# Optimization experiments

Measured on AMD Instinct MI355X. Metric: run time of the kernel, lower is better.

Reference implementation:

```python
import jax, jax.numpy as jnp
import numpy as np

B, S, D = 4, 2048, 1024

def setup_inputs() -> dict:
    key = jax.random.key(0)
    kx, kq, kk, kv = jax.random.split(key, 4)
    glorot = (6.0 / (D + D)) ** 0.5
    return {
        "x": jax.random.normal(kx, (B, S, D), dtype=jnp.float32),
        "Wq": jax.random.uniform(kq, (D, D), jnp.float32, -glorot, glorot),
        "Wk": jax.random.uniform(kk, (D, D), jnp.float32, -glorot, glorot),
        "Wv": jax.random.uniform(kv, (D, D), jnp.float32, -glorot, glorot),
    }

def reference(x, Wq, Wk, Wv):
    # q,k,v: [B,S,D]
    q = jnp.einsum("bsd,de->bse", x, Wq)
    k = jnp.einsum("bsd,de->bse", x, Wk)
    v = jnp.einsum("bsd,de->bse", x, Wv)
    scale = jnp.sqrt(jnp.asarray(q.shape[-1], q.dtype))
    scores = jnp.einsum("bqd,bkd->bqk", q, k) / scale  # [B,S,S]
    w = jax.nn.softmax(scores, axis=-1)
    return jnp.einsum("bqk,bkd->bqd", w, v)
```

## Files before the change

kernel.cpp:

```cpp
#include <hip/hip_runtime.h>
#include <hip/hip_bf16.h>


typedef _Float16 half_t;
typedef _Float16 half8 __attribute__((ext_vector_type(8)));
typedef _Float16 half4v __attribute__((ext_vector_type(4)));
typedef float f32x4 __attribute__((ext_vector_type(4)));

__device__ __forceinline__ void load16_to_lds(const half_t* g, half_t* l) {
  __builtin_amdgcn_global_load_lds(
      (const __attribute__((address_space(1))) void*)g,
      (__attribute__((address_space(3))) void*)l, 16, 0, 0);
}

__global__ __launch_bounds__(512, 2) void qkvt_gemm8(
    const half_t* __restrict__ xh, const half_t* __restrict__ wt,
    half_t* __restrict__ qk, half_t* __restrict__ vtg) {
  __shared__ __align__(16) half_t As[2][256 * 64];
  __shared__ __align__(16) half_t Bs[2][256 * 64];

  int b = blockIdx.x;
  const half_t* A; const half_t* Bm; half_t* C;
  int ldc, m0, n0;
  if (b < 256) {
    A = xh; Bm = wt; C = qk; ldc = 2048;
    m0 = (b >> 3) * 256; n0 = (b & 7) * 256;
  } else {
    b -= 256;
    A = wt + (size_t)2 * 1024 * 1024; Bm = xh; C = vtg; ldc = 8192;
    m0 = (b >> 5) * 256; n0 = (b & 31) * 256;
  }

  const int t     = threadIdx.x;
  const int lane  = t & 63;
  const int wave  = t >> 6;
  const int wr128 = (wave >> 2) * 128;
  const int wc64  = (wave & 3) * 64;
  const int lm    = lane & 15;
  const int lq    = lane >> 4;
  const int pos0  = (lq ^ (lm & 7)) * 8;
  const int pos1  = ((4 + lq) ^ (lm & 7)) * 8;
  const int t8    = t * 8;

  const int trow = t >> 3;
  const int tchk = (t & 7) ^ (trow & 7);
  const half_t* gA0 = A  + (size_t)(m0 + trow) * 1024 + tchk * 8;
  const half_t* gB0 = Bm + (size_t)(n0 + trow) * 1024 + tchk * 8;

  f32x4 acc[8][4] = {};
  half8 va[4][2], vb0[2][2], vb1[2][2];

#define ST_A(buf, h, kt) do {                                                  \
    load16_to_lds(gA0 + (size_t)((h)*128) * 1024 + (size_t)(kt) * 64,          \
                  &As[buf][(h)*128*64] + t8);                                  \
    load16_to_lds(gA0 + (size_t)((h)*128+64) * 1024 + (size_t)(kt) * 64,       \
                  &As[buf][((h)*128+64)*64] + t8);                             \
  } while (0)
#define ST_B(buf, h, kt) do {                                                  \
    load16_to_lds(gB0 + (size_t)((h)*128) * 1024 + (size_t)(kt) * 64,          \
                  &Bs[buf][(h)*128*64] + t8);                                  \
    load16_to_lds(gB0 + (size_t)((h)*128+64) * 1024 + (size_t)(kt) * 64,       \
                  &Bs[buf][((h)*128+64)*64] + t8);                             \
  } while (0)
#define RD_A(buf, mh) do {                                                     \
    _Pragma("unroll") for (int m = 0; m < 4; ++m) {                            \
      const int ar = wr128 + (mh)*64 + m * 16 + lm;                            \
      va[m][0] = *(const half8*)&As[buf][ar * 64 + pos0];                      \
      va[m][1] = *(const half8*)&As[buf][ar * 64 + pos1];                      \
    } } while (0)
#define RD_B(buf, nh, vb) do {                                                 \
    _Pragma("unroll") for (int n = 0; n < 2; ++n) {                            \
      const int br = wc64 + (nh)*32 + n * 16 + lm;                             \
      vb[n][0] = *(const half8*)&Bs[buf][br * 64 + pos0];                      \
      vb[n][1] = *(const half8*)&Bs[buf][br * 64 + pos1];                      \
    } } while (0)
#define MF_Q(mh, nh, vb) do {                                                  \
    _Pragma("unroll") for (int kk = 0; kk < 2; ++kk)                           \
    _Pragma("unroll") for (int m = 0; m < 4; ++m)                              \
    _Pragma("unroll") for (int n = 0; n < 2; ++n)                              \
      acc[(mh)*4+m][(nh)*2+n] = __builtin_amdgcn_mfma_f32_16x16x32_f16(        \
          va[m][kk], vb[n][kk], acc[(mh)*4+m][(nh)*2+n], 0, 0, 0);             \
  } while (0)
#define LGKM0 asm volatile("s_waitcnt lgkmcnt(0)" ::: "memory")
#define BAR   __builtin_amdgcn_s_barrier()
#define PRIO1 __builtin_amdgcn_s_setprio(1)
#define PRIO0 __builtin_amdgcn_s_setprio(0)

  ST_A(0, 0, 0); ST_A(0, 1, 0);
  ST_B(0, 0, 0); ST_B(0, 1, 0);
  ST_B(1, 0, 1); ST_B(1, 1, 1);
  asm volatile("s_waitcnt vmcnt(4)" ::: "memory");
  BAR;

#pragma unroll 1
  for (int i = 0; i < 8; ++i) {
    const int st1 = (2 * i + 1 < 15) ? 2 * i + 1 : 15;
    const int st2 = (2 * i + 2 < 15) ? 2 * i + 2 : 15;
    const int st3 = (2 * i + 3 < 15) ? 2 * i + 3 : 15;
    RD_A(0, 0); RD_B(0, 0, vb0);
    ST_A(1, 0, st1);
    asm volatile("s_waitcnt lgkmcnt(8)" ::: "memory");
    BAR; LGKM0;
    PRIO1; MF_Q(0, 0, vb0); PRIO0;
    BAR;
    RD_B(0, 1, vb1);
    ST_A(1, 1, st1);
    BAR; LGKM0;
    PRIO1; MF_Q(0, 1, vb1); PRIO0;
    BAR;
    RD_A(0, 1);
    ST_B(0, 0, st2);
    BAR; LGKM0;
    PRIO1; MF_Q(1, 0, vb0); PRIO0;
    BAR;
    ST_B(0, 1, st2);
    BAR; LGKM0;
    PRIO1; MF_Q(1, 1, vb1); PRIO0;
    asm volatile("s_waitcnt vmcnt(4)" ::: "memory");
    BAR;
    RD_A(1, 0); RD_B(1, 0, vb0);
    ST_A(0, 0, st2);
    asm volatile("s_waitcnt lgkmcnt(8)" ::: "memory");
    BAR; LGKM0;
    PRIO1; MF_Q(0, 0, vb0); PRIO0;
    BAR;
    RD_B(1, 1, vb1);
    ST_A(0, 1, st2);
    BAR; LGKM0;
    PRIO1; MF_Q(0, 1, vb1); PRIO0;
    BAR;
    RD_A(1, 1);
    ST_B(1, 0, st3);
    BAR; LGKM0;
    PRIO1; MF_Q(1, 0, vb0); PRIO0;
    BAR;
    ST_B(1, 1, st3);
    BAR; LGKM0;
    PRIO1; MF_Q(1, 1, vb1); PRIO0;
    asm volatile("s_waitcnt vmcnt(4)" ::: "memory");
    BAR;
  }

#pragma unroll
  for (int m = 0; m < 8; ++m)
#pragma unroll
    for (int n = 0; n < 4; ++n) {
      const int col = n0 + wc64 + n * 16 + lm;
#pragma unroll
      for (int r = 0; r < 4; ++r) {
        const int row = m0 + wr128 + m * 16 + lq * 4 + r;
        C[(size_t)row * ldc + col] = (half_t)acc[m][n][r];
      }
    }
#undef ST_A
#undef ST_B
#undef RD_A
#undef RD_B
#undef MF_Q
#undef LGKM0
#undef BAR
#undef PRIO1
#undef PRIO0
}

__global__ __launch_bounds__(256) void scores_gemm(
    const half_t* __restrict__ qk, half_t* __restrict__ sc,
    float* __restrict__ lpart) {
  __shared__ __align__(16) half_t As[128 * 64];
  __shared__ __align__(16) half_t Bs[128 * 64];

  const int z  = blockIdx.z;
  const int m0 = blockIdx.y * 128;
  const int n0 = blockIdx.x * 128;
  const half_t* A  = qk + (size_t)z * 2048 * 2048;
  const half_t* Bm = A + 1024;
  half_t* C = sc + (size_t)z * 2048 * 2048;
  constexpr int lda = 2048, ldb = 2048, ldc = 2048, K = 1024;

  const int t    = threadIdx.x;
  const int wave = t >> 6;
  const int lane = t & 63;
  const int wm   = (wave >> 1) * 64;
  const int wn   = (wave & 1) * 64;
  const int lm   = lane & 15;
  const int lq   = lane >> 4;
  const int lswz = lm & 7;

  const int trow = t >> 3;
  const int tchk = (t & 7) ^ (trow & 7);

  const half_t* gA0 = A  + (size_t)(m0 + trow) * lda + tchk * 8;
  const half_t* gB0 = Bm + (size_t)(n0 + trow) * ldb + tchk * 8;
  const size_t stepA = (size_t)32 * lda;
  const size_t stepB = (size_t)32 * ldb;

  half_t* lA0 = &As[t * 8];
  half_t* lB0 = &Bs[t * 8];

  f32x4 acc[4][4] = {};

  for (int k0 = 0; k0 < K; k0 += 64) {
    __syncthreads();
#pragma unroll
    for (int n = 0; n < 4; ++n) {
      load16_to_lds(gA0 + n * stepA + k0, lA0 + n * 2048);
      load16_to_lds(gB0 + n * stepB + k0, lB0 + n * 2048);
    }
    __syncthreads();

#pragma unroll
    for (int kk = 0; kk < 2; ++kk) {
      const int pos = ((kk * 4 + lq) ^ lswz) * 8;
      half8 a[4], bf[4];
#pragma unroll
      for (int i = 0; i < 4; ++i)
        a[i] = *(const half8*)&As[(wm + i * 16 + lm) * 64 + pos];
#pragma unroll
      for (int j = 0; j < 4; ++j)
        bf[j] = *(const half8*)&Bs[(wn + j * 16 + lm) * 64 + pos];
#pragma unroll
      for (int i = 0; i < 4; ++i)
#pragma unroll
        for (int j = 0; j < 4; ++j)
          acc[i][j] = __builtin_amdgcn_mfma_f32_16x16x32_f16(a[i], bf[j], acc[i][j], 0, 0, 0);
    }
  }

  const float scale = 1.0f / 32.0f;
#pragma unroll
  for (int i = 0; i < 4; ++i)
#pragma unroll
    for (int r = 0; r < 4; ++r) {
      const int row = m0 + wm + i * 16 + lq * 4 + r;
      float s = 0.f;
#pragma unroll
      for (int j = 0; j < 4; ++j) {
        const int col = n0 + wn + j * 16 + lm;
        float v = __expf(acc[i][j][r] * scale - 8.0f);
        s += v;
        C[(size_t)row * ldc + col] = (half_t)v;
      }
      s += __shfl_xor(s, 1); s += __shfl_xor(s, 2);
      s += __shfl_xor(s, 4); s += __shfl_xor(s, 8);
      if (lm == 0)
        lpart[((size_t)z * 2048 + row) * 32 + blockIdx.x * 2 + (wave & 1)] = s;
    }
}

__global__ __launch_bounds__(256) void pv_gemm(
    const half_t* __restrict__ sc, const half_t* __restrict__ vtg,
    float* __restrict__ out, const float* __restrict__ lpart) {
  __shared__ __align__(16) half_t As[128 * 64];
  __shared__ __align__(16) half_t Bs[128 * 64];
  __shared__ float linv[128];

  const int z  = blockIdx.z;
  const int m0 = blockIdx.x * 128;
  const int n0 = blockIdx.y * 128;
  const half_t* A  = sc  + (size_t)z * 2048 * 2048;
  const half_t* Bm = vtg + (size_t)z * 2048;
  float* C = out + (size_t)z * 2048 * 1024;
  constexpr int lda = 2048, ldb = 8192, ldc = 1024, K = 2048;

  const int t    = threadIdx.x;
  const int wave = t >> 6;
  const int lane = t & 63;
  const int wm   = (wave >> 1) * 64;
  const int wn   = (wave & 1) * 64;
  const int lm   = lane & 15;
  const int lq   = lane >> 4;
  const int lswz = lm & 7;

  if (t < 128) {
    const float4* lp = (const float4*)&lpart[((size_t)z * 2048 + m0 + t) * 32];
    float s = 0.f;
#pragma unroll
    for (int p = 0; p < 8; ++p) {
      float4 v = lp[p];
      s += v.x + v.y + v.z + v.w;
    }
    linv[t] = 1.0f / s;
  }

  const int trow = t >> 3;
  const int tchk = (t & 7) ^ (trow & 7);

  const half_t* gA0 = A  + (size_t)(m0 + trow) * lda + tchk * 8;
  const half_t* gB0 = Bm + (size_t)(n0 + trow) * ldb + tchk * 8;
  const size_t stepA = (size_t)32 * lda;
  const size_t stepB = (size_t)32 * ldb;

  half_t* lA0 = &As[t * 8];
  half_t* lB0 = &Bs[t * 8];

  f32x4 acc[4][4] = {};

  for (int k0 = 0; k0 < K; k0 += 64) {
    __syncthreads();
#pragma unroll
    for (int n = 0; n < 4; ++n) {
      load16_to_lds(gA0 + n * stepA + k0, lA0 + n * 2048);
      load16_to_lds(gB0 + n * stepB + k0, lB0 + n * 2048);
    }
    __syncthreads();

#pragma unroll
    for (int kk = 0; kk < 2; ++kk) {
      const int pos = ((kk * 4 + lq) ^ lswz) * 8;
      half8 a[4], bf[4];
#pragma unroll
      for (int i = 0; i < 4; ++i)
        a[i] = *(const half8*)&As[(wm + i * 16 + lm) * 64 + pos];
#pragma unroll
      for (int j = 0; j < 4; ++j)
        bf[j] = *(const half8*)&Bs[(wn + j * 16 + lm) * 64 + pos];
#pragma unroll
      for (int i = 0; i < 4; ++i)
#pragma unroll
        for (int j = 0; j < 4; ++j)
          acc[i][j] = __builtin_amdgcn_mfma_f32_16x16x32_f16(a[i], bf[j], acc[i][j], 0, 0, 0);
    }
  }

#pragma unroll
  for (int i = 0; i < 4; ++i)
#pragma unroll
    for (int r = 0; r < 4; ++r) {
      const int lrow = wm + i * 16 + lq * 4 + r;
      const float inv = linv[lrow];
      const int row = m0 + lrow;
#pragma unroll
      for (int j = 0; j < 4; ++j) {
        const int col = n0 + wn + j * 16 + lm;
        C[(size_t)row * ldc + col] = acc[i][j][r] * inv;
      }
    }
}

__global__ __launch_bounds__(256) void prep(
    const float* __restrict__ x, half_t* __restrict__ xh,
    const float* __restrict__ Wq, const float* __restrict__ Wk,
    const float* __restrict__ Wv, half_t* __restrict__ wt) {
  __shared__ half_t tile[32][33];
  const int b = blockIdx.x;
  const int t = threadIdx.x;
  if (b < 8192) {
    const int i = (b * 256 + t) * 4;
    const float4 v = *reinterpret_cast<const float4*>(x + i);
    half4v o;
    o.x = (half_t)v.x; o.y = (half_t)v.y; o.z = (half_t)v.z; o.w = (half_t)v.w;
    *reinterpret_cast<half4v*>(xh + i) = o;
  } else {
    int bb = b - 8192;
    const int w = bb >> 10; bb &= 1023;
    const float* in = (w == 0) ? Wq : (w == 1) ? Wk : Wv;
    half_t* o = wt + (size_t)w * 1024 * 1024;
    const int r0 = (bb >> 5) * 32, c0 = (bb & 31) * 32;
    const int tx = t & 31, ty = t >> 5;
#pragma unroll
    for (int i = 0; i < 32; i += 8)
      tile[ty + i][tx] = (half_t)in[(size_t)(r0 + ty + i) * 1024 + c0 + tx];
    __syncthreads();
#pragma unroll
    for (int i = 0; i < 32; i += 8)
      o[(size_t)(c0 + ty + i) * 1024 + r0 + tx] = tile[tx][ty + i];
  }
}

extern "C" void kernel_launch(void* const* d_in, const int* in_sizes, int n_in,
                              void* d_out, int out_size, void* d_ws, size_t ws_size,
                              hipStream_t stream) {
  constexpr int Bb = 4, S = 2048, D = 1024;
  constexpr size_t MS = (size_t)Bb * S;

  const float* x  = (const float*)d_in[0];
  const float* Wq = (const float*)d_in[1];
  const float* Wk = (const float*)d_in[2];
  const float* Wv = (const float*)d_in[3];
  float* out = (float*)d_out;

  char* p = (char*)d_ws;
  half_t* xh    = (half_t*)p; p += MS * D * 2;
  half_t* wt    = (half_t*)p; p += (size_t)3 * D * D * 2;
  half_t* qk    = (half_t*)p; p += MS * (size_t)(2 * D) * 2;
  half_t* vtg   = (half_t*)p; p += (size_t)D * MS * 2;
  half_t* sc    = (half_t*)p; p += (size_t)Bb * S * S * 2;
  float*  lpart = (float*)p;  p += MS * 32 * 4;

  prep<<<11264, 256, 0, stream>>>(x, xh, Wq, Wk, Wv, wt);
  qkvt_gemm8<<<384, 512, 0, stream>>>(xh, wt, qk, vtg);
  scores_gemm<<<dim3(16, 16, Bb), 256, 0, stream>>>(qk, sc, lpart);
  pv_gemm<<<dim3(16, 8, Bb), 256, 0, stream>>>(sc, vtg, out, lpart);
}
```

Baseline: 242.6 us.

## Port scores GEMM to 256x256 pipelined 8-wave kernel and remap block order

Replaces the simple 128x128 single-buffered scores GEMM with the same 256x256-tile, 512-thread, double-buffered, barrier-interleaved MFMA pipeline already used for the QKV projection. It also remaps block indices in both GEMMs so that consecutive blocks fall into groups sharing operand tiles, which should improve L2 and cache locality across XCDs. The larger tile raises data reuse and overlaps global-to-LDS loads with MFMA work. In exchange there are fewer blocks (256), so the GPU may be less evenly loaded, and the lpart partial-sum indexing changes to 4 waves per 256-column tile, which pv_gemm must still read correctly.

```diff
diff --git a/kernel.cpp b/kernel.cpp
--- a/kernel.cpp
+++ b/kernel.cpp
@@ -12,6 +12,13 @@
       (const __attribute__((address_space(1))) void*)g,
       (__attribute__((address_space(3))) void*)l, 16, 0, 0);
 }
+
+#define LGKM0 asm volatile("s_waitcnt lgkmcnt(0)" ::: "memory")
+#define LGKM8 asm volatile("s_waitcnt lgkmcnt(8)" ::: "memory")
+#define VM4   asm volatile("s_waitcnt vmcnt(4)" ::: "memory")
+#define BAR   __builtin_amdgcn_s_barrier()
+#define PRIO1 __builtin_amdgcn_s_setprio(1)
+#define PRIO0 __builtin_amdgcn_s_setprio(0)
 
 __global__ __launch_bounds__(512, 2) void qkvt_gemm8(
     const half_t* __restrict__ xh, const half_t* __restrict__ wt,
@@ -19,16 +26,20 @@
   __shared__ __align__(16) half_t As[2][256 * 64];
   __shared__ __align__(16) half_t Bs[2][256 * 64];
 
-  int b = blockIdx.x;
+  const int b = blockIdx.x;
   const half_t* A; const half_t* Bm; half_t* C;
   int ldc, m0, n0;
   if (b < 256) {
+    const int x = b & 7, j = b >> 3;
     A = xh; Bm = wt; C = qk; ldc = 2048;
-    m0 = (b >> 3) * 256; n0 = (b & 7) * 256;
+    m0 = (x * 4 + (j & 3)) * 256;
+    n0 = (j >> 2) * 256;
   } else {
-    b -= 256;
+    const int idv = b - 256;
+    const int x = idv & 7, j = idv >> 3;
     A = wt + (size_t)2 * 1024 * 1024; Bm = xh; C = vtg; ldc = 8192;
-    m0 = (b >> 5) * 256; n0 = (b & 31) * 256;
+    m0 = (j >> 2) * 256;
+    n0 = (x * 4 + (j & 3)) * 256;
   }
 
   const int t     = threadIdx.x;
@@ -81,15 +92,11 @@
       acc[(mh)*4+m][(nh)*2+n] = __builtin_amdgcn_mfma_f32_16x16x32_f16(        \
           va[m][kk], vb[n][kk], acc[(mh)*4+m][(nh)*2+n], 0, 0, 0);             \
   } while (0)
-#define LGKM0 asm volatile("s_waitcnt lgkmcnt(0)" ::: "memory")
-#define BAR   __builtin_amdgcn_s_barrier()
-#define PRIO1 __builtin_amdgcn_s_setprio(1)
-#define PRIO0 __builtin_amdgcn_s_setprio(0)
 
   ST_A(0, 0, 0); ST_A(0, 1, 0);
   ST_B(0, 0, 0); ST_B(0, 1, 0);
   ST_B(1, 0, 1); ST_B(1, 1, 1);
-  asm volatile("s_waitcnt vmcnt(4)" ::: "memory");
+  VM4;
   BAR;
 
 #pragma unroll 1
@@ -99,7 +106,7 @@
     const int st3 = (2 * i + 3 < 15) ? 2 * i + 3 : 15;
     RD_A(0, 0); RD_B(0, 0, vb0);
     ST_A(1, 0, st1);
-    asm volatile("s_waitcnt lgkmcnt(8)" ::: "memory");
+    LGKM8;
     BAR; LGKM0;
     PRIO1; MF_Q(0, 0, vb0); PRIO0;
     BAR;
@@ -116,11 +123,11 @@
     ST_B(0, 1, st2);
     BAR; LGKM0;
     PRIO1; MF_Q(1, 1, vb1); PRIO0;
-    asm volatile("s_waitcnt vmcnt(4)" ::: "memory");
+    VM4;
     BAR;
     RD_A(1, 0); RD_B(1, 0, vb0);
     ST_A(0, 0, st2);
-    asm volatile("s_waitcnt lgkmcnt(8)" ::: "memory");
+    LGKM8;
     BAR; LGKM0;
     PRIO1; MF_Q(0, 0, vb0); PRIO0;
     BAR;
@@ -137,7 +144,7 @@
     ST_B(1, 1, st3);
     BAR; LGKM0;
     PRIO1; MF_Q(1, 1, vb1); PRIO0;
-    asm volatile("s_waitcnt vmcnt(4)" ::: "memory");
+    VM4;
     BAR;
   }
 
@@ -157,94 +164,155 @@
 #undef RD_A
 #undef RD_B
 #undef MF_Q
-#undef LGKM0
-#undef BAR
-#undef PRIO1
-#undef PRIO0
-}
-
-__global__ __launch_bounds__(256) void scores_gemm(
+}
+
+__global__ __launch_bounds__(512, 2) void scores_gemm8(
     const half_t* __restrict__ qk, half_t* __restrict__ sc,
     float* __restrict__ lpart) {
-  __shared__ __align__(16) half_t As[128 * 64];
-  __shared__ __align__(16) half_t Bs[128 * 64];
-
-  const int z  = blockIdx.z;
-  const int m0 = blockIdx.y * 128;
-  const int n0 = blockIdx.x * 128;
+  __shared__ __align__(16) half_t As[2][256 * 64];
+  __shared__ __align__(16) half_t Bs[2][256 * 64];
+
+  const int id  = blockIdx.x;
+  const int x   = id & 7, j = id >> 3;
+  const int bx  = j & 7;
+  const int z   = x >> 1;
+  const int by  = (x & 1) * 4 + (j >> 3);
+  const int m0  = by * 256;
+  const int n0  = bx * 256;
   const half_t* A  = qk + (size_t)z * 2048 * 2048;
   const half_t* Bm = A + 1024;
   half_t* C = sc + (size_t)z * 2048 * 2048;
-  constexpr int lda = 2048, ldb = 2048, ldc = 2048, K = 1024;
-
-  const int t    = threadIdx.x;
-  const int wave = t >> 6;
-  const int lane = t & 63;
-  const int wm   = (wave >> 1) * 64;
-  const int wn   = (wave & 1) * 64;
-  const int lm   = lane & 15;
-  const int lq   = lane >> 4;
-  const int lswz = lm & 7;
+
+  const int t     = threadIdx.x;
+  const int lane  = t & 63;
+  const int wave  = t >> 6;
+  const int wr128 = (wave >> 2) * 128;
+  const int wc64  = (wave & 3) * 64;
+  const int lm    = lane & 15;
+  const int lq    = lane >> 4;
+  const int pos0  = (lq ^ (lm & 7)) * 8;
+  const int pos1  = ((4 + lq) ^ (lm & 7)) * 8;
+  const int t8    = t * 8;
 
   const int trow = t >> 3;
   const int tchk = (t & 7) ^ (trow & 7);
-
-  const half_t* gA0 = A  + (size_t)(m0 + trow) * lda + tchk * 8;
-  const half_t* gB0 = Bm + (size_t)(n0 + trow) * ldb + tchk * 8;
-  const size_t stepA = (size_t)32 * lda;
-  const size_t stepB = (size_t)32 * ldb;
-
-  half_t* lA0 = &As[t * 8];
-  half_t* lB0 = &Bs[t * 8];
-
-  f32x4 acc[4][4] = {};
-
-  for (int k0 = 0; k0 < K; k0 += 64) {
-    __syncthreads();
-#pragma unroll
-    for (int n = 0; n < 4; ++n) {
-      load16_to_lds(gA0 + n * stepA + k0, lA0 + n * 2048);
-      load16_to_lds(gB0 + n * stepB + k0, lB0 + n * 2048);
-    }
-    __syncthreads();
-
-#pragma unroll
-    for (int kk = 0; kk < 2; ++kk) {
-      const int pos = ((kk * 4 + lq) ^ lswz) * 8;
-      half8 a[4], bf[4];
-#pragma unroll
-      for (int i = 0; i < 4; ++i)
-        a[i] = *(const half8*)&As[(wm + i * 16 + lm) * 64 + pos];
-#pragma unroll
-      for (int j = 0; j < 4; ++j)
-        bf[j] = *(const half8*)&Bs[(wn + j * 16 + lm) * 64 + pos];
-#pragma unroll
-      for (int i = 0; i < 4; ++i)
-#pragma unroll
-        for (int j = 0; j < 4; ++j)
-          acc[i][j] = __builtin_amdgcn_mfma_f32_16x16x32_f16(a[i], bf[j], acc[i][j], 0, 0, 0);
-    }
+  const half_t* gA0 = A  + (size_t)(m0 + trow) * 2048 + tchk * 8;
+  const half_t* gB0 = Bm + (size_t)(n0 + trow) * 2048 + tchk * 8;
+
+  f32x4 acc[8][4] = {};
+  half8 va[4][2], vb0[2][2], vb1[2][2];
+
+#define ST_A(buf, h, kt) do {                                                  \
+    load16_to_lds(gA0 + (size_t)((h)*128) * 2048 + (size_t)(kt) * 64,          \
+                  &As[buf][(h)*128*64] + t8);                                  \
+    load16_to_lds(gA0 + (size_t)((h)*128+64) * 2048 + (size_t)(kt) * 64,       \
+                  &As[buf][((h)*128+64)*64] + t8);                             \
+  } while (0)
+#define ST_B(buf, h, kt) do {                                                  \
+    load16_to_lds(gB0 + (size_t)((h)*128) * 2048 + (size_t)(kt) * 64,          \
+                  &Bs[buf][(h)*128*64] + t8);                                  \
+    load16_to_lds(gB0 + (size_t)((h)*128+64) * 2048 + (size_t)(kt) * 64,       \
+                  &Bs[buf][((h)*128+64)*64] + t8);                             \
+  } while (0)
+#define RD_A(buf, mh) do {                                                     \
+    _Pragma("unroll") for (int m = 0; m < 4; ++m) {                            \
+      const int ar = wr128 + (mh)*64 + m * 16 + lm;                            \
+      va[m][0] = *(const half8*)&As[buf][ar * 64 + pos0];                      \
+      va[m][1] = *(const half8*)&As[buf][ar * 64 + pos1];                      \
+    } } while (0)
+#define RD_B(buf, nh, vb) do {                                                 \
+    _Pragma("unroll") for (int n = 0; n < 2; ++n) {                            \
+      const int br = wc64 + (nh)*32 + n * 16 + lm;                             \
+      vb[n][0] = *(const half8*)&Bs[buf][br * 64 + pos0];                      \
+      vb[n][1] = *(const half8*)&Bs[buf][br * 64 + pos1];                      \
+    } } while (0)
+#define MF_Q(mh, nh, vb) do {                                                  \
+    _Pragma("unroll") for (int kk = 0; kk < 2; ++kk)                           \
+    _Pragma("unroll") for (int m = 0; m < 4; ++m)                              \
+    _Pragma("unroll") for (int n = 0; n < 2; ++n)                              \
+      acc[(mh)*4+m][(nh)*2+n] = __builtin_amdgcn_mfma_f32_16x16x32_f16(        \
+          va[m][kk], vb[n][kk], acc[(mh)*4+m][(nh)*2+n], 0, 0, 0);             \
+  } while (0)
+
+  ST_A(0, 0, 0); ST_A(0, 1, 0);
+  ST_B(0, 0, 0); ST_B(0, 1, 0);
+  ST_B(1, 0, 1); ST_B(1, 1, 1);
+  VM4;
+  BAR;
+
+#pragma unroll 1
+  for (int i = 0; i < 8; ++i) {
+    const int st1 = (2 * i + 1 < 15) ? 2 * i + 1 : 15;
+    const int st2 = (2 * i + 2 < 15) ? 2 * i + 2 : 15;
+    const int st3 = (2 * i + 3 < 15) ? 2 * i + 3 : 15;
+    RD_A(0, 0); RD_B(0, 0, vb0);
+    ST_A(1, 0, st1);
+    LGKM8;
+    BAR; LGKM0;
+    PRIO1; MF_Q(0, 0, vb0); PRIO0;
+    BAR;
+    RD_B(0, 1, vb1);
+    ST_A(1, 1, st1);
+    BAR; LGKM0;
+    PRIO1; MF_Q(0, 1, vb1); PRIO0;
+    BAR;
+    RD_A(0, 1);
+    ST_B(0, 0, st2);
+    BAR; LGKM0;
+    PRIO1; MF_Q(1, 0, vb0); PRIO0;
+    BAR;
+    ST_B(0, 1, st2);
+    BAR; LGKM0;
+    PRIO1; MF_Q(1, 1, vb1); PRIO0;
+    VM4;
+    BAR;
+    RD_A(1, 0); RD_B(1, 0, vb0);
+    ST_A(0, 0, st2);
+    LGKM8;
+    BAR; LGKM0;
+    PRIO1; MF_Q(0, 0, vb0); PRIO0;
+    BAR;
+    RD_B(1, 1, vb1);
+    ST_A(0, 1, st2);
+    BAR; LGKM0;
+    PRIO1; MF_Q(0, 1, vb1); PRIO0;
+    BAR;
+    RD_A(1, 1);
+    ST_B(1, 0, st3);
+    BAR; LGKM0;
+    PRIO1; MF_Q(1, 0, vb0); PRIO0;
+    BAR;
+    ST_B(1, 1, st3);
+    BAR; LGKM0;
+    PRIO1; MF_Q(1, 1, vb1); PRIO0;
+    VM4;
+    BAR;
   }
 
   const float scale = 1.0f / 32.0f;
 #pragma unroll
-  for (int i = 0; i < 4; ++i)
+  for (int m = 0; m < 8; ++m)
 #pragma unroll
     for (int r = 0; r < 4; ++r) {
-      const int row = m0 + wm + i * 16 + lq * 4 + r;
+      const int row = m0 + wr128 + m * 16 + lq * 4 + r;
       float s = 0.f;
 #pragma unroll
-      for (int j = 0; j < 4; ++j) {
-        const int col = n0 + wn + j * 16 + lm;
-        float v = __expf(acc[i][j][r] * scale - 8.0f);
+      for (int n = 0; n < 4; ++n) {
+        const int col = n0 + wc64 + n * 16 + lm;
+        float v = __expf(acc[m][n][r] * scale - 8.0f);
         s += v;
-        C[(size_t)row * ldc + col] = (half_t)v;
+        C[(size_t)row * 2048 + col] = (half_t)v;
       }
       s += __shfl_xor(s, 1); s += __shfl_xor(s, 2);
       s += __shfl_xor(s, 4); s += __shfl_xor(s, 8);
       if (lm == 0)
-        lpart[((size_t)z * 2048 + row) * 32 + blockIdx.x * 2 + (wave & 1)] = s;
-    }
+        lpart[((size_t)z * 2048 + row) * 32 + bx * 4 + (wave & 3)] = s;
+    }
+#undef ST_A
+#undef ST_B
+#undef RD_A
+#undef RD_B
+#undef MF_Q
 }
 
 __global__ __launch_bounds__(256) void pv_gemm(
@@ -389,6 +457,6 @@
 
   prep<<<11264, 256, 0, stream>>>(x, xh, Wq, Wk, Wv, wt);
   qkvt_gemm8<<<384, 512, 0, stream>>>(xh, wt, qk, vtg);
-  scores_gemm<<<dim3(16, 16, Bb), 256, 0, stream>>>(qk, sc, lpart);
+  scores_gemm8<<<256, 512, 0, stream>>>(qk, sc, lpart);
   pv_gemm<<<dim3(16, 8, Bb), 256, 0, stream>>>(sc, vtg, out, lpart);
 }
```

New measurement: 236.5 us. 2.5% less time.
